# Kernel optimization log

Hardware: AMD Instinct MI355X
Metric: run time of the kernel (lower is better)

Reference implementation:

```python
import jax, jax.numpy as jnp
import numpy as np

H, W = 512, 512          # cart_size
HP, WP = 64, 2048        # polar_size
DROP = 3.0               # center_drop_grid_size
B, C = 4, 64


def _build_grids():
    # Mirrors Polar2Cart.__init__ (mode='in') exactly.
    yy, xx = np.meshgrid(np.arange(H, dtype=np.float32), np.arange(W, dtype=np.float32), indexing='ij')
    yyc = yy - H / 2.0 + 0.5
    xxc = xx - W / 2.0 + 0.5
    depth = np.sqrt(xxc ** 2 + yyc ** 2)
    phi = np.pi - np.arctan2(yyc, xxc)
    index_y = depth / (H / 2.0 * np.sqrt(2.0)) * (HP + DROP) - DROP
    index_x = phi / np.pi / 2.0 * WP
    mask = (index_y > 0).reshape(-1)
    gy = (index_y / HP * 2.0 - 1.0).reshape(-1)[mask]
    gx = (index_x / WP * 2.0 - 1.0).reshape(-1)[mask]
    iy = yy.reshape(-1)[mask].astype(np.int32)
    ix = xx.reshape(-1)[mask].astype(np.int32)
    # torch code stacks (index_x, -index_y) as (x, y) grid coords
    return gx.astype(np.float32), (-gy).astype(np.float32), iy, ix


def setup_inputs() -> dict:
    key = jax.random.key(0)
    k1, k2 = jax.random.split(key)
    gx, gy, iy, ix = _build_grids()
    return {
        'polar_feat': jax.random.normal(k1, (B, C, HP, WP), jnp.float32),
        'ref_feat': jax.random.normal(k2, (B, C, H, W), jnp.float32),
        'grid_x': jnp.asarray(gx),
        'grid_y': jnp.asarray(gy),
        'idx_y': jnp.asarray(iy),
        'idx_x': jnp.asarray(ix),
    }


def _bilinear_sample(feat, gx, gy):
    # feat: [B,C,Hp,Wp]; gx,gy: [N] normalized coords.
    # torch F.grid_sample(mode='bilinear', padding_mode='zeros', align_corners=True)
    Hp, Wp = feat.shape[2], feat.shape[3]
    ixf = (gx + 1.0) * (Wp - 1) * 0.5
    iyf = (gy + 1.0) * (Hp - 1) * 0.5
    x0 = jnp.floor(ixf)
    y0 = jnp.floor(iyf)
    wx1 = ixf - x0
    wy1 = iyf - y0
    out = jnp.zeros((feat.shape[0], feat.shape[1], gx.shape[0]), feat.dtype)
    for dy, wy in ((0, 1.0 - wy1), (1, wy1)):
        for dx, wx in ((0, 1.0 - wx1), (1, wx1)):
            xi = x0 + dx
            yi = y0 + dy
            valid = (xi >= 0) & (xi < Wp) & (yi >= 0) & (yi < Hp)
            xc = jnp.clip(xi, 0, Wp - 1).astype(jnp.int32)
            yc = jnp.clip(yi, 0, Hp - 1).astype(jnp.int32)
            w = jnp.where(valid, wx * wy, 0.0).astype(feat.dtype)
            out = out + feat[:, :, yc, xc] * w  # [B,C,N]
    return out


def reference(polar_feat, ref_feat, grid_x, grid_y, idx_y, idx_x):
    Bc, Cc = ref_feat.shape[0], ref_feat.shape[1]
    N = idx_y.shape[0]
    sampled = _bilinear_sample(polar_feat, grid_x, grid_y)      # [B,C,N]
    vals = sampled.transpose(0, 2, 1).reshape(Bc * N, Cc)       # permute(0,2,1,3).reshape(-1,C)
    b_idx = jnp.repeat(jnp.arange(Bc, dtype=jnp.int32), N)
    out = ref_feat.at[b_idx, :, jnp.tile(idx_y, Bc), jnp.tile(idx_x, Bc)].set(vals)
    return out
```

## Files before the change

### kernel.cpp

```cpp
#include <hip/hip_runtime.h>

#define HH  512
#define WW  512
#define HPP 64
#define WPP 2048
#define BB  4
#define CC  64

__global__ __launch_bounds__(256) void fill_disk(
    const float* __restrict__ ref, float* __restrict__ out) {
    int t  = blockIdx.x * 256 + threadIdx.x;
    int bc = blockIdx.y;
    int r = 240 + (t >> 5);
    int c = 240 + (t & 31);
    float yyc = (float)r - 255.5f;
    float xxc = (float)c - 255.5f;
    float depth = sqrtf(yyc * yyc + xxc * xxc);
    float iyv = depth * (67.0f / 362.03867196751236f) - 3.0f;
    if (iyv <= 1e-3f) {
        size_t off = (size_t)bc * (HH * WW) + (size_t)r * WW + c;
        out[off] = ref[off];
    }
}

struct __attribute__((packed, aligned(4))) fpair { float lo, hi; };

__global__ __launch_bounds__(256) void sample_scatter(
    const float* __restrict__ polar,
    const float* __restrict__ gx, const float* __restrict__ gy,
    const int* __restrict__ idx_y, const int* __restrict__ idx_x,
    float* __restrict__ out, int N) {
    int nwg = gridDim.x;
    int bid = blockIdx.x;
    int q = nwg >> 3, r = nwg & 7;
    int xcd = bid & 7, lid = bid >> 3;
    int swz = (xcd < r ? xcd * (q + 1) : r * (q + 1) + (xcd - r) * q) + lid;

    int n = swz * 256 + (int)threadIdx.x;
    if (n >= N) return;
    int b = blockIdx.y;

    float gxv = gx[n], gyv = gy[n];
    float ixf = (gxv + 1.0f) * ((WPP - 1) * 0.5f);
    float iyf = (gyv + 1.0f) * ((HPP - 1) * 0.5f);
    float x0f = floorf(ixf), y0f = floorf(iyf);
    float wx1 = ixf - x0f,  wy1 = iyf - y0f;
    float wx0 = 1.0f - wx1, wy0 = 1.0f - wy1;
    int x0 = (int)x0f, y0 = (int)y0f;
    int x1 = x0 + 1,   y1 = y0 + 1;

    bool vx0 = (x0 >= 0) & (x0 < WPP);
    bool vx1 = (x1 >= 0) & (x1 < WPP);
    bool vy0 = (y0 >= 0) & (y0 < HPP);
    bool vy1 = (y1 >= 0) & (y1 < HPP);
    float w00 = (vx0 && vy0) ? wx0 * wy0 : 0.0f;
    float w01 = (vx1 && vy0) ? wx1 * wy0 : 0.0f;
    float w10 = (vx0 && vy1) ? wx0 * wy1 : 0.0f;
    float w11 = (vx1 && vy1) ? wx1 * wy1 : 0.0f;

    int xs  = min(max(x0, 0), WPP - 2);
    int ys0 = min(max(y0, 0), HPP - 1);
    int ys1 = min(max(y1, 0), HPP - 1);

    int oy = idx_y[n], ox = idx_x[n];

    const char* pb = (const char*)polar + (size_t)b * ((size_t)CC * HPP * WPP * 4);
    char*       ob = (char*)out + (size_t)b * ((size_t)CC * HH * WW * 4)
                               + (size_t)(oy * WW + ox) * 4;
    unsigned offA = (unsigned)(ys0 * WPP + xs) * 4u;
    unsigned offB = (unsigned)(ys1 * WPP + xs) * 4u;

    #pragma unroll 8
    for (int c = 0; c < CC; ++c) {
        fpair a01 = *(const fpair*)(pb + offA);
        fpair b01 = *(const fpair*)(pb + offB);
        float v = a01.lo * w00 + a01.hi * w01 + b01.lo * w10 + b01.hi * w11;
        __builtin_nontemporal_store(v, (float*)ob);
        pb += (size_t)HPP * WPP * 4;
        ob += (size_t)HH * WW * 4;
    }
}

extern "C" void kernel_launch(void* const* d_in, const int* in_sizes, int n_in,
                              void* d_out, int out_size, void* d_ws, size_t ws_size,
                              hipStream_t stream) {
    const float* polar = (const float*)d_in[0];
    const float* ref   = (const float*)d_in[1];
    const float* gxp   = (const float*)d_in[2];
    const float* gyp   = (const float*)d_in[3];
    const int*   iyp   = (const int*)d_in[4];
    const int*   ixp   = (const int*)d_in[5];
    float* out = (float*)d_out;
    int N = in_sizes[2];

    fill_disk<<<dim3(4, BB * CC), 256, 0, stream>>>(ref, out);
    sample_scatter<<<dim3((N + 255) / 256, BB), 256, 0, stream>>>(
        polar, gxp, gyp, iyp, ixp, out, N);
}
```

Baseline: 581.3 us.

## Scatter grid into dense 2D map and sample with 16x16 spatial tiles

```diff
diff --git a/kernel.cpp b/kernel.cpp
--- a/kernel.cpp
+++ b/kernel.cpp
@@ -23,18 +23,82 @@
     }
 }
 
+__global__ __launch_bounds__(256) void scatter_map(
+    const float* __restrict__ gx, const float* __restrict__ gy,
+    const int* __restrict__ idx_y, const int* __restrict__ idx_x,
+    float2* __restrict__ map, int N) {
+    int n = blockIdx.x * 256 + threadIdx.x;
+    if (n >= N) return;
+    map[idx_y[n] * WW + idx_x[n]] = make_float2(gx[n], gy[n]);
+}
+
 struct __attribute__((packed, aligned(4))) fpair { float lo, hi; };
 
-__global__ __launch_bounds__(256) void sample_scatter(
+__global__ __launch_bounds__(256) void sample_tiled(
+    const float* __restrict__ polar, const float2* __restrict__ map,
+    float* __restrict__ out) {
+    int bid = blockIdx.x;
+    int swz = ((bid & 7) << 7) + (bid >> 3);
+    int tile_r = swz >> 5, tile_c = swz & 31;
+
+    int t = (int)threadIdx.x;
+    int wave = t >> 6, lane = t & 63;
+    int r = tile_r * 16 + ((wave >> 1) << 3) + (lane >> 3);
+    int c = tile_c * 16 + ((wave & 1) << 3) + (lane & 7);
+
+    float2 mv = map[r * WW + c];
+    if (!(mv.x > -2.0f)) return;
+    int b = blockIdx.y;
+
+    float gxv = mv.x, gyv = mv.y;
+    float ixf = (gxv + 1.0f) * ((WPP - 1) * 0.5f);
+    float iyf = (gyv + 1.0f) * ((HPP - 1) * 0.5f);
+    float x0f = floorf(ixf), y0f = floorf(iyf);
+    float wx1 = ixf - x0f,  wy1 = iyf - y0f;
+    float wx0 = 1.0f - wx1, wy0 = 1.0f - wy1;
+    int x0 = (int)x0f, y0 = (int)y0f;
+    int x1 = x0 + 1,   y1 = y0 + 1;
+
+    bool vx0 = (x0 >= 0) & (x0 < WPP);
+    bool vx1 = (x1 >= 0) & (x1 < WPP);
+    bool vy0 = (y0 >= 0) & (y0 < HPP);
+    bool vy1 = (y1 >= 0) & (y1 < HPP);
+    float w00 = (vx0 && vy0) ? wx0 * wy0 : 0.0f;
+    float w01 = (vx1 && vy0) ? wx1 * wy0 : 0.0f;
+    float w10 = (vx0 && vy1) ? wx0 * wy1 : 0.0f;
+    float w11 = (vx1 && vy1) ? wx1 * wy1 : 0.0f;
+
+    int xs  = min(max(x0, 0), WPP - 2);
+    int ys0 = min(max(y0, 0), HPP - 1);
+    int ys1 = min(max(y1, 0), HPP - 1);
+
+    const char* pb = (const char*)polar + (size_t)b * ((size_t)CC * HPP * WPP * 4);
+    char*       ob = (char*)out + (size_t)b * ((size_t)CC * HH * WW * 4)
+                               + (size_t)(r * WW + c) * 4;
+    unsigned offA = (unsigned)(ys0 * WPP + xs) * 4u;
+    unsigned offB = (unsigned)(ys1 * WPP + xs) * 4u;
+
+    #pragma unroll 8
+    for (int ch = 0; ch < CC; ++ch) {
+        fpair a01 = *(const fpair*)(pb + offA);
+        fpair b01 = *(const fpair*)(pb + offB);
+        float v = a01.lo * w00 + a01.hi * w01 + b01.lo * w10 + b01.hi * w11;
+        *(float*)ob = v;
+        pb += (size_t)HPP * WPP * 4;
+        ob += (size_t)HH * WW * 4;
+    }
+}
+
+__global__ __launch_bounds__(256) void sample_scatter_v2(
     const float* __restrict__ polar,
     const float* __restrict__ gx, const float* __restrict__ gy,
     const int* __restrict__ idx_y, const int* __restrict__ idx_x,
     float* __restrict__ out, int N) {
     int nwg = gridDim.x;
     int bid = blockIdx.x;
-    int q = nwg >> 3, r = nwg & 7;
+    int q = nwg >> 3, rr = nwg & 7;
     int xcd = bid & 7, lid = bid >> 3;
-    int swz = (xcd < r ? xcd * (q + 1) : r * (q + 1) + (xcd - r) * q) + lid;
+    int swz = (xcd < rr ? xcd * (q + 1) : rr * (q + 1) + (xcd - rr) * q) + lid;
 
     int n = swz * 256 + (int)threadIdx.x;
     if (n >= N) return;
@@ -63,7 +127,6 @@
     int ys1 = min(max(y1, 0), HPP - 1);
 
     int oy = idx_y[n], ox = idx_x[n];
-
     const char* pb = (const char*)polar + (size_t)b * ((size_t)CC * HPP * WPP * 4);
     char*       ob = (char*)out + (size_t)b * ((size_t)CC * HH * WW * 4)
                                + (size_t)(oy * WW + ox) * 4;
@@ -71,7 +134,7 @@
     unsigned offB = (unsigned)(ys1 * WPP + xs) * 4u;
 
     #pragma unroll 8
-    for (int c = 0; c < CC; ++c) {
+    for (int ch = 0; ch < CC; ++ch) {
         fpair a01 = *(const fpair*)(pb + offA);
         fpair b01 = *(const fpair*)(pb + offB);
         float v = a01.lo * w00 + a01.hi * w01 + b01.lo * w10 + b01.hi * w11;
@@ -93,7 +156,18 @@
     float* out = (float*)d_out;
     int N = in_sizes[2];
 
+    const size_t map_bytes = (size_t)HH * WW * sizeof(float2);
+
     fill_disk<<<dim3(4, BB * CC), 256, 0, stream>>>(ref, out);
-    sample_scatter<<<dim3((N + 255) / 256, BB), 256, 0, stream>>>(
-        polar, gxp, gyp, iyp, ixp, out, N);
+
+    if (ws_size >= map_bytes) {
+        float2* map = (float2*)d_ws;
+        hipMemsetAsync(map, 0xFF, map_bytes, stream);
+        scatter_map<<<dim3((N + 255) / 256), 256, 0, stream>>>(
+            gxp, gyp, iyp, ixp, map, N);
+        sample_tiled<<<dim3(1024, BB), 256, 0, stream>>>(polar, map, out);
+    } else {
+        sample_scatter_v2<<<dim3((N + 255) / 256, BB), 256, 0, stream>>>(
+            polar, gxp, gyp, iyp, ixp, out, N);
+    }
 }
```

Result: slower. 610.7 us (+5.0%).
